# Kernel optimization log

Measured on AMD Instinct MI355X. Metric: run time of the kernel, lower is better.

The kernel has to match this reference:

```python
import jax, jax.numpy as jnp
import numpy as np

N_NODES = 100000
N_EDGES = 1600000
D = 128
RESIDUAL_WEIGHT = 0.001


def setup_inputs() -> dict:
    key = jax.random.key(0)
    k = jax.random.split(key, 7)
    x = jax.random.normal(k[0], (N_NODES, D), dtype=jnp.float32)
    edge_index = jax.random.randint(k[1], (2, N_EDGES), 0, N_NODES, dtype=jnp.int32)
    s = 1.0 / np.sqrt(D)
    Wl = jax.random.normal(k[2], (D, D), dtype=jnp.float32) * s
    bl = jax.random.normal(k[3], (D,), dtype=jnp.float32) * s
    Wr = jax.random.normal(k[4], (D, D), dtype=jnp.float32) * s
    Wres = jax.random.normal(k[5], (D, D), dtype=jnp.float32) * s
    bres = jax.random.normal(k[6], (D,), dtype=jnp.float32) * s
    return {"x": x, "edge_index": edge_index, "Wl": Wl, "bl": bl,
            "Wr": Wr, "Wres": Wres, "bres": bres}


def reference(x, edge_index, Wl, bl, Wr, Wres, bres):
    # PyG SAGEConv(aggr='sum'): messages x_j flow src -> dst
    src, dst = edge_index[0], edge_index[1]
    agg = jax.ops.segment_sum(x[src], dst, num_segments=x.shape[0])  # [N, D]
    # lin_l(agg) (with bias) + lin_r(x) (root weight, no bias)
    h_sage = agg @ Wl.T + bl + x @ Wr.T
    # residual Linear
    h_res = x @ Wres.T + bres
    rw = jnp.float32(RESIDUAL_WEIGHT)
    # dropout p=0 (eval) -> identity
    return rw * h_sage + (1.0 - rw) * h_res
```

## Files before the change

### kernel.cpp

```cpp
#include <hip/hip_runtime.h>
#include <hip/hip_bf16.h>
#include <stdint.h>

#define DD 128
#define RW 0.001f
#define CHUNK 4096
#define CAP 4096
#define YS 8.0f

#if defined(__has_builtin)
#if __has_builtin(__builtin_amdgcn_cvt_scalef32_pk_fp4_f32) && __has_builtin(__builtin_amdgcn_cvt_scalef32_pk_f32_fp4)
#define HAVE_FP4 1
#endif
#endif
#ifndef HAVE_FP4
#define HAVE_FP4 0
#endif

#if HAVE_FP4
#define XBB 64
#else
#define XBB 128
#endif

typedef __attribute__((ext_vector_type(4))) float f32x4;
typedef __attribute__((ext_vector_type(2))) float f32x2;
typedef __attribute__((ext_vector_type(8))) short bf16x8;

static __device__ __forceinline__ uint32_t pack2(float lo, float hi){
  return __builtin_amdgcn_perm(__float_as_uint(hi), __float_as_uint(lo), 0x07060302u);
}

static __device__ __forceinline__ ushort rne_bf16(float f){
  uint32_t u = __float_as_uint(f);
  return (ushort)((u + 0x7fffu + ((u >> 16) & 1u)) >> 16);
}

__global__ __launch_bounds__(512) void fused_prep(
    const int* __restrict__ src, const int* __restrict__ dst,
    int* __restrict__ gcnt, uint32_t* __restrict__ recs, int E, int nb, int nchunk,
    const float* __restrict__ x, uint8_t* __restrict__ xb, int n8, int nq, int M,
    const float* __restrict__ Wl, const float* __restrict__ bl,
    const float* __restrict__ Wr, const float* __restrict__ Wres,
    const float* __restrict__ bres, ushort* __restrict__ Wfb, float* __restrict__ bc)
{
  __shared__ uint32_t srec[CHUNK];
  __shared__ uint16_t sb[CHUNK];
  __shared__ int hcnt[800];
  __shared__ int hbase[800];
  __shared__ int lcur[800];
  int t = threadIdx.x;
  int b = blockIdx.x;

  if (b < nchunk){
    int base = b * CHUNK;
    for (int i = t; i < nb; i += 512){ hcnt[i] = 0; lcur[i] = 0; }
    __syncthreads();
    #pragma unroll
    for (int k = 0; k < 8; k++){
      int idx = k * 512 + t;
      int e = base + idx;
      uint16_t bb = 0xFFFFu;
      if (e < E){
        int d = dst[e];
        bb = (uint16_t)(d >> 7);
        srec[idx] = ((uint32_t)(d & 127) << 17) | (uint32_t)src[e];
        atomicAdd(&hcnt[bb], 1);
      }
      sb[idx] = bb;
    }
    __syncthreads();
    for (int i = t; i < nb; i += 512)
      hbase[i] = hcnt[i] ? atomicAdd(&gcnt[i], hcnt[i]) : 0;
    __syncthreads();
    #pragma unroll
    for (int k = 0; k < 8; k++){
      int idx = k * 512 + t;
      uint16_t bb = sb[idx];
      if (bb != 0xFFFFu){
        int p = hbase[bb] + atomicAdd(&lcur[bb], 1);
        if (p < CAP) recs[(size_t)bb * CAP + p] = srec[idx];
      }
    }
  } else if (b < nchunk + nq){
    int i = (b - nchunk) * 512 + t;
    if (i < n8){
      const f32x4* p = (const f32x4*)(x + (size_t)i * 8);
      f32x4 f0 = p[0], f1 = p[1];
#if HAVE_FP4
      uint32_t d = 0;
      d = __builtin_amdgcn_cvt_scalef32_pk_fp4_f32(d, f0[0], f0[1], 1.0f, 0);
      d = __builtin_amdgcn_cvt_scalef32_pk_fp4_f32(d, f0[2], f0[3], 1.0f, 1);
      d = __builtin_amdgcn_cvt_scalef32_pk_fp4_f32(d, f1[0], f1[1], 1.0f, 2);
      d = __builtin_amdgcn_cvt_scalef32_pk_fp4_f32(d, f1[2], f1[3], 1.0f, 3);
      *(uint32_t*)(xb + (size_t)i * 4) = d;
#else
      int pk0 = __builtin_amdgcn_cvt_pk_fp8_f32(f0[0], f0[1], 0, false);
      pk0     = __builtin_amdgcn_cvt_pk_fp8_f32(f0[2], f0[3], pk0, true);
      int pk1 = __builtin_amdgcn_cvt_pk_fp8_f32(f1[0], f1[1], 0, false);
      pk1     = __builtin_amdgcn_cvt_pk_fp8_f32(f1[2], f1[3], pk1, true);
      uint2 w; w.x = (uint32_t)pk0; w.y = (uint32_t)pk1;
      *(uint2*)(xb + (size_t)i * 8) = w;
#endif
    }
  } else {
    int i = (b - nchunk - nq) * 512 + t;
    if (i < 8 && i * 16 < XBB){
      uint4 z = {0u, 0u, 0u, 0u};
      *(uint4*)(xb + (size_t)M * XBB + i * 16) = z;
    }
    if (i < DD * 256){
      int c = i >> 8, k = i & 255;
      float v;
      if (k < DD) v = RW * Wr[c * DD + k] + (1.f - RW) * Wres[c * DD + k];
      else        v = (RW / YS) * Wl[c * DD + (k - DD)];
      Wfb[i] = rne_bf16(v);
      if (i < DD) bc[i] = RW * bl[i] + (1.f - RW) * bres[i];
    }
  }
}

__global__ __launch_bounds__(512) void bsort(uint32_t* __restrict__ recs,
                                             const int* __restrict__ gcnt,
                                             int2* __restrict__ meta, int M){
  __shared__ uint32_t srec[CAP];
  __shared__ uint32_t ssorted[CAP];
  __shared__ int h[128], pstart[128], lc[128];
  int t = threadIdx.x;
  int b = blockIdx.x;
  int s = b * CAP;
  int cnt = gcnt[b];
  if (cnt > CAP) cnt = CAP;

  if (t < 128){ h[t] = 0; lc[t] = 0; }
  __syncthreads();
  for (int i = t; i < cnt; i += 512){
    uint32_t r = recs[s + i];
    srec[i] = r;
    atomicAdd(&h[(r >> 17) & 127u], 1);
  }
  __syncthreads();
  int val = (t < 128) ? h[t] : 0;
  #pragma unroll
  for (int off = 1; off < 128; off <<= 1){
    if (t < 128) pstart[t] = val;
    __syncthreads();
    if (t < 128 && t >= off) val += pstart[t - off];
    __syncthreads();
  }
  if (t < 128){
    pstart[t] = val - h[t];
    int node = b * 128 + t;
    if (node < M) meta[node] = make_int2(s + pstart[t], h[t]);
  }
  __syncthreads();
  for (int i = t; i < cnt; i += 512){
    uint32_t r = srec[i];
    int n7 = (int)((r >> 17) & 127u);
    int pos = pstart[n7] + atomicAdd(&lc[n7], 1);
    ssorted[pos] = r & 0x1FFFFu;
  }
  __syncthreads();
  for (int i = t; i < cnt; i += 512)
    recs[s + i] = ssorted[i];
}

__global__ __launch_bounds__(256) void agg(const uint8_t* __restrict__ xb,
                                           const uint32_t* __restrict__ csr,
                                           const int2* __restrict__ meta,
                                           uint8_t* __restrict__ ybar, int N)
{
  int wid = (int)((blockIdx.x * 256 + threadIdx.x) >> 6);
  if (wid >= N) return;
  int lane = threadIdx.x & 63;
  int2 mc = meta[wid];
  int start = mc.x, cnt = mc.y;
  uint32_t raw = csr[start + lane];
  uint32_t vidx = (lane < cnt) ? raw : (uint32_t)N;

  f32x2 acc[8];
  #pragma unroll
  for (int k = 0; k < 8; k++) acc[k] = (f32x2){0.f, 0.f};

#if HAVE_FP4
  int voff = lane;
#else
  int voff = lane * 2;
#endif

  int n64 = cnt < 64 ? cnt : 64;
  int nit = (n64 + 15) >> 4;
  for (int it = 0; it < nit; it++){
    int bb = it << 4;
    #pragma unroll
    for (int k = 0; k < 16; k++){
      uint32_t s = (uint32_t)__builtin_amdgcn_readlane((int)vidx, bb + k);
#if HAVE_FP4
      int v = *(const uint8_t*)(xb + (size_t)s * XBB + voff);
      f32x2 f = __builtin_amdgcn_cvt_scalef32_pk_f32_fp4(v, 1.0f, 0);
#else
      int v = *(const ushort*)(xb + (size_t)s * XBB + voff);
      f32x2 f = __builtin_amdgcn_cvt_pk_f32_fp8(v, false);
#endif
      acc[k & 7] += f;
    }
  }
  for (int j = 64; j < cnt; j++){
    uint32_t s = csr[start + j];
#if HAVE_FP4
    int v = *(const uint8_t*)(xb + (size_t)s * XBB + voff);
    f32x2 f = __builtin_amdgcn_cvt_scalef32_pk_f32_fp4(v, 1.0f, 0);
#else
    int v = *(const ushort*)(xb + (size_t)s * XBB + voff);
    f32x2 f = __builtin_amdgcn_cvt_pk_f32_fp8(v, false);
#endif
    acc[0] += f;
  }

  f32x2 r = (acc[0] + acc[1]) + (acc[2] + acc[3]) + ((acc[4] + acc[5]) + (acc[6] + acc[7]));
  float a0 = r[0] * YS, a1 = r[1] * YS;
  int pk = __builtin_amdgcn_cvt_pk_fp8_f32(a0, a1, 0, false);
  *(ushort*)(ybar + (size_t)wid * DD + lane * 2) = (ushort)(pk & 0xFFFF);
}

__global__ __launch_bounds__(512, 4) void gemm2(
    const float* __restrict__ x, const uint8_t* __restrict__ ybar,
    const ushort* __restrict__ Wfb, const float* __restrict__ bc,
    float* __restrict__ out, int M)
{
  __shared__ char sX[32768];
  int tid = threadIdx.x;
  int lane = tid & 63, w = tid >> 6;
  int wr = w >> 2, wcol = w & 3;
  int l15 = lane & 15, lhi = lane >> 4;
  int rowbase = blockIdx.x * 128 + wr * 64;
  int colbase = wcol * 32;

  f32x4 acc[4][2];
  #pragma unroll
  for (int a = 0; a < 4; a++)
    #pragma unroll
    for (int b = 0; b < 2; b++) acc[a][b] = (f32x4){0.f,0.f,0.f,0.f};

  #pragma unroll
  for (int p = 0; p < 4; p++){
    int g   = p * 512 + tid;
    int row = g >> 4;
    int cx  = tid & 15;
    int grow = blockIdx.x * 128 + row;
    if (grow >= M) grow = M - 1;
    const float* ap = x + (size_t)grow * DD + cx * 8;
    f32x4 f0 = *(const f32x4*)ap;
    f32x4 f1 = *(const f32x4*)(ap + 4);
    uint4 wv;
    wv.x = pack2(f0[0], f0[1]);
    wv.y = pack2(f0[2], f0[3]);
    wv.z = pack2(f1[0], f1[1]);
    wv.w = pack2(f1[2], f1[3]);
    int sw = (row << 8) | ((cx * 16) ^ ((row & 7) << 4));
    *(uint4*)&sX[sw] = wv;
  }
  __syncthreads();

  #pragma unroll
  for (int ks = 0; ks < 4; ks++){
    bf16x8 afr[4];
    #pragma unroll
    for (int rt = 0; rt < 4; rt++){
      int row = wr * 64 + rt * 16 + l15;
      int byte = (row << 8) | ((ks * 64 + lhi * 16) ^ ((row & 7) << 4));
      afr[rt] = *(const bf16x8*)&sX[byte];
    }
    #pragma unroll
    for (int ct = 0; ct < 2; ct++){
      int colm = colbase + ct * 16 + l15;
      bf16x8 bfr = *(const bf16x8*)(Wfb + (size_t)colm * 256 + ks * 32 + lhi * 8);
      #pragma unroll
      for (int rt = 0; rt < 4; rt++)
        acc[rt][ct] = __builtin_amdgcn_mfma_f32_16x16x32_bf16(bfr, afr[rt], acc[rt][ct], 0, 0, 0);
    }
  }
  __syncthreads();

  #pragma unroll
  for (int p = 0; p < 4; p++){
    int g   = p * 512 + tid;
    int row = g >> 4;
    int cx  = tid & 15;
    int grow = blockIdx.x * 128 + row;
    if (grow >= M) grow = M - 1;
    uint2 rv = *(const uint2*)(ybar + (size_t)grow * DD + cx * 8);
    f32x2 e0 = __builtin_amdgcn_cvt_pk_f32_fp8((int)rv.x, false);
    f32x2 e1 = __builtin_amdgcn_cvt_pk_f32_fp8((int)rv.x, true);
    f32x2 e2 = __builtin_amdgcn_cvt_pk_f32_fp8((int)rv.y, false);
    f32x2 e3 = __builtin_amdgcn_cvt_pk_f32_fp8((int)rv.y, true);
    uint4 wv;
    wv.x = pack2(e0[0], e0[1]);
    wv.y = pack2(e1[0], e1[1]);
    wv.z = pack2(e2[0], e2[1]);
    wv.w = pack2(e3[0], e3[1]);
    int sw = (row << 8) | ((cx * 16) ^ ((row & 7) << 4));
    *(uint4*)&sX[sw] = wv;
  }
  __syncthreads();

  #pragma unroll
  for (int ks = 0; ks < 4; ks++){
    bf16x8 afr[4];
    #pragma unroll
    for (int rt = 0; rt < 4; rt++){
      int row = wr * 64 + rt * 16 + l15;
      int byte = (row << 8) | ((ks * 64 + lhi * 16) ^ ((row & 7) << 4));
      afr[rt] = *(const bf16x8*)&sX[byte];
    }
    #pragma unroll
    for (int ct = 0; ct < 2; ct++){
      int colm = colbase + ct * 16 + l15;
      bf16x8 bfr = *(const bf16x8*)(Wfb + (size_t)colm * 256 + 128 + ks * 32 + lhi * 8);
      #pragma unroll
      for (int rt = 0; rt < 4; rt++)
        acc[rt][ct] = __builtin_amdgcn_mfma_f32_16x16x32_bf16(bfr, afr[rt], acc[rt][ct], 0, 0, 0);
    }
  }

  #pragma unroll
  for (int ct = 0; ct < 2; ct++){
    int col = colbase + ct * 16 + lhi * 4;
    f32x4 b4 = *(const f32x4*)&bc[col];
    #pragma unroll
    for (int rt = 0; rt < 4; rt++){
      int row = rowbase + rt * 16 + l15;
      if (row < M){
        f32x4 o = acc[rt][ct] + b4;
        *(f32x4*)(out + (size_t)row * DD + col) = o;
      }
    }
  }
}

extern "C" void kernel_launch(void* const* d_in, const int* in_sizes, int n_in,
                              void* d_out, int out_size, void* d_ws, size_t ws_size,
                              hipStream_t stream) {
  const float* x    = (const float*)d_in[0];
  const int*   ei   = (const int*)d_in[1];
  const float* Wl   = (const float*)d_in[2];
  const float* bl   = (const float*)d_in[3];
  const float* Wr   = (const float*)d_in[4];
  const float* Wres = (const float*)d_in[5];
  const float* bres = (const float*)d_in[6];
  float* out = (float*)d_out;

  int M = in_sizes[0] / DD;
  int E = in_sizes[1] / 2;
  const int* esrc = ei;
  const int* edst = ei + E;
  int nb = (M + 127) >> 7;

  char* wsp = (char*)d_ws;
  size_t off = 0;
  uint8_t*  xb   = (uint8_t*) (wsp + off); off += (size_t)(M + 1) * 128; off = (off + 255) & ~255ull;
  uint8_t*  ybar = (uint8_t*) (wsp + off); off += (size_t)M * DD;        off = (off + 255) & ~255ull;
  uint32_t* recs = (uint32_t*)(wsp + off); off += (size_t)800 * CAP * 4;
  ushort*   Wfb  = (ushort*)  (wsp + off); off += DD * 256 * 2;
  float*    bc   = (float*)   (wsp + off); off += 512;
  int*      gcnt = (int*)     (wsp + off); off += sizeof(int) * 1024;
  int2*     meta = (int2*)    (wsp + off); off += sizeof(int2) * (size_t)M;

  int n8 = M * 16;
  int nchunk = (E + CHUNK - 1) / CHUNK;
  int nq = (n8 + 511) / 512;
  int nprep = (DD * 256 + 511) / 512;

  hipMemsetAsync(gcnt, 0, sizeof(int) * 1024, stream);
  fused_prep<<<nchunk + nq + nprep, 512, 0, stream>>>(
      esrc, edst, gcnt, recs, E, nb, nchunk,
      x, xb, n8, nq, M,
      Wl, bl, Wr, Wres, bres, Wfb, bc);
  bsort<<<nb, 512, 0, stream>>>(recs, gcnt, meta, M);
  agg<<<((size_t)M * 64 + 255) / 256, 256, 0, stream>>>(xb, recs, meta, ybar, M);
  gemm2<<<(M + 127) / 128, 512, 0, stream>>>(x, ybar, Wfb, bc, out, M);
}
```

Before: 111.2 us.

## Fuse neighbor aggregation into the GEMM kernel, dropping the fp8 ybar buffer

The separate aggregation kernel is removed. Each GEMM block now gathers neighbor sums for its own 128 nodes directly into shared memory as bf16, with each wave handling 16 nodes and prefetching the next node's CSR entries. This removes a kernel launch and the write-then-read round trip of the fp8 ybar intermediate, along with its YS scaling. The cost is that gather latency now runs inside the GEMM block, with fewer waves per node and only two accumulators instead of eight. Occupancy hints are raised to 6 blocks per CU to help hide that latency.

```diff
diff --git a/kernel.cpp b/kernel.cpp
--- a/kernel.cpp
+++ b/kernel.cpp
@@ -6,7 +6,6 @@
 #define RW 0.001f
 #define CHUNK 4096
 #define CAP 4096
-#define YS 8.0f
 
 #if defined(__has_builtin)
 #if __has_builtin(__builtin_amdgcn_cvt_scalef32_pk_fp4_f32) && __has_builtin(__builtin_amdgcn_cvt_scalef32_pk_f32_fp4)
@@ -113,7 +112,7 @@
       int c = i >> 8, k = i & 255;
       float v;
       if (k < DD) v = RW * Wr[c * DD + k] + (1.f - RW) * Wres[c * DD + k];
-      else        v = (RW / YS) * Wl[c * DD + (k - DD)];
+      else        v = RW * Wl[c * DD + (k - DD)];
       Wfb[i] = rne_bf16(v);
       if (i < DD) bc[i] = RW * bl[i] + (1.f - RW) * bres[i];
     }
@@ -165,72 +164,76 @@
     recs[s + i] = ssorted[i];
 }
 
-__global__ __launch_bounds__(256) void agg(const uint8_t* __restrict__ xb,
-                                           const uint32_t* __restrict__ csr,
-                                           const int2* __restrict__ meta,
-                                           uint8_t* __restrict__ ybar, int N)
-{
-  int wid = (int)((blockIdx.x * 256 + threadIdx.x) >> 6);
-  if (wid >= N) return;
-  int lane = threadIdx.x & 63;
-  int2 mc = meta[wid];
-  int start = mc.x, cnt = mc.y;
-  uint32_t raw = csr[start + lane];
-  uint32_t vidx = (lane < cnt) ? raw : (uint32_t)N;
-
-  f32x2 acc[8];
-  #pragma unroll
-  for (int k = 0; k < 8; k++) acc[k] = (f32x2){0.f, 0.f};
-
-#if HAVE_FP4
-  int voff = lane;
-#else
-  int voff = lane * 2;
-#endif
-
-  int n64 = cnt < 64 ? cnt : 64;
-  int nit = (n64 + 15) >> 4;
-  for (int it = 0; it < nit; it++){
-    int bb = it << 4;
-    #pragma unroll
-    for (int k = 0; k < 16; k++){
-      uint32_t s = (uint32_t)__builtin_amdgcn_readlane((int)vidx, bb + k);
-#if HAVE_FP4
-      int v = *(const uint8_t*)(xb + (size_t)s * XBB + voff);
-      f32x2 f = __builtin_amdgcn_cvt_scalef32_pk_f32_fp4(v, 1.0f, 0);
-#else
-      int v = *(const ushort*)(xb + (size_t)s * XBB + voff);
-      f32x2 f = __builtin_amdgcn_cvt_pk_f32_fp8(v, false);
-#endif
-      acc[k & 7] += f;
-    }
-  }
-  for (int j = 64; j < cnt; j++){
-    uint32_t s = csr[start + j];
-#if HAVE_FP4
-    int v = *(const uint8_t*)(xb + (size_t)s * XBB + voff);
-    f32x2 f = __builtin_amdgcn_cvt_scalef32_pk_f32_fp4(v, 1.0f, 0);
-#else
-    int v = *(const ushort*)(xb + (size_t)s * XBB + voff);
-    f32x2 f = __builtin_amdgcn_cvt_pk_f32_fp8(v, false);
-#endif
-    acc[0] += f;
-  }
-
-  f32x2 r = (acc[0] + acc[1]) + (acc[2] + acc[3]) + ((acc[4] + acc[5]) + (acc[6] + acc[7]));
-  float a0 = r[0] * YS, a1 = r[1] * YS;
-  int pk = __builtin_amdgcn_cvt_pk_fp8_f32(a0, a1, 0, false);
-  *(ushort*)(ybar + (size_t)wid * DD + lane * 2) = (ushort)(pk & 0xFFFF);
-}
-
-__global__ __launch_bounds__(512, 4) void gemm2(
-    const float* __restrict__ x, const uint8_t* __restrict__ ybar,
+__global__ __launch_bounds__(512, 6) void gemm_agg(
+    const float* __restrict__ x, const uint8_t* __restrict__ xb,
+    const uint32_t* __restrict__ csr, const int2* __restrict__ meta,
     const ushort* __restrict__ Wfb, const float* __restrict__ bc,
     float* __restrict__ out, int M)
 {
   __shared__ char sX[32768];
   int tid = threadIdx.x;
   int lane = tid & 63, w = tid >> 6;
+
+  {
+    int nodebase = blockIdx.x * 128 + w * 16;
+    int mrow = nodebase + (lane & 15);
+    int2 mpre = (mrow < M) ? meta[mrow] : make_int2(0, 0);
+
+    int start = __builtin_amdgcn_readlane(mpre.x, 0);
+    int cnt   = __builtin_amdgcn_readlane(mpre.y, 0);
+    uint32_t vidx = csr[start + lane];
+    vidx = (lane < cnt) ? vidx : (uint32_t)M;
+
+    for (int j = 0; j < 16; j++){
+      int start_n = 0, cnt_n = 0;
+      uint32_t vidx_n = (uint32_t)M;
+      if (j < 15){
+        start_n = __builtin_amdgcn_readlane(mpre.x, j + 1);
+        cnt_n   = __builtin_amdgcn_readlane(mpre.y, j + 1);
+        uint32_t rawn = csr[start_n + lane];
+        vidx_n = (lane < cnt_n) ? rawn : (uint32_t)M;
+      }
+
+      f32x2 acc0 = (f32x2){0.f, 0.f}, acc1 = (f32x2){0.f, 0.f};
+      int n64 = cnt < 64 ? cnt : 64;
+      int nit = (n64 + 15) >> 4;
+      for (int it = 0; it < nit; it++){
+        int bb = it << 4;
+        #pragma unroll
+        for (int k = 0; k < 16; k++){
+          uint32_t s = (uint32_t)__builtin_amdgcn_readlane((int)vidx, bb + k);
+#if HAVE_FP4
+          int v = *(const uint8_t*)(xb + (size_t)s * XBB + lane);
+          f32x2 f = __builtin_amdgcn_cvt_scalef32_pk_f32_fp4(v, 1.0f, 0);
+#else
+          int v = *(const ushort*)(xb + (size_t)s * XBB + lane * 2);
+          f32x2 f = __builtin_amdgcn_cvt_pk_f32_fp8(v, false);
+#endif
+          if (k & 1) acc1 += f; else acc0 += f;
+        }
+      }
+      for (int t2 = 64; t2 < cnt; t2++){
+        uint32_t s = csr[start + t2];
+#if HAVE_FP4
+        int v = *(const uint8_t*)(xb + (size_t)s * XBB + lane);
+        f32x2 f = __builtin_amdgcn_cvt_scalef32_pk_f32_fp4(v, 1.0f, 0);
+#else
+        int v = *(const ushort*)(xb + (size_t)s * XBB + lane * 2);
+        f32x2 f = __builtin_amdgcn_cvt_pk_f32_fp8(v, false);
+#endif
+        acc0 += f;
+      }
+      f32x2 acc = acc0 + acc1;
+
+      int row = w * 16 + j;
+      int sw = (row << 8) | ((lane * 4) ^ ((row & 7) << 4));
+      *(uint32_t*)&sX[sw] = pack2(acc[0], acc[1]);
+
+      start = start_n; cnt = cnt_n; vidx = vidx_n;
+    }
+  }
+  __syncthreads();
+
   int wr = w >> 2, wcol = w & 3;
   int l15 = lane & 15, lhi = lane >> 4;
   int rowbase = blockIdx.x * 128 + wr * 64;
@@ -241,6 +244,26 @@
   for (int a = 0; a < 4; a++)
     #pragma unroll
     for (int b = 0; b < 2; b++) acc[a][b] = (f32x4){0.f,0.f,0.f,0.f};
+
+  #pragma unroll
+  for (int ks = 0; ks < 4; ks++){
+    bf16x8 afr[4];
+    #pragma unroll
+    for (int rt = 0; rt < 4; rt++){
+      int row = wr * 64 + rt * 16 + l15;
+      int byte = (row << 8) | ((ks * 64 + lhi * 16) ^ ((row & 7) << 4));
+      afr[rt] = *(const bf16x8*)&sX[byte];
+    }
+    #pragma unroll
+    for (int ct = 0; ct < 2; ct++){
+      int colm = colbase + ct * 16 + l15;
+      bf16x8 bfr = *(const bf16x8*)(Wfb + (size_t)colm * 256 + 128 + ks * 32 + lhi * 8);
+      #pragma unroll
+      for (int rt = 0; rt < 4; rt++)
+        acc[rt][ct] = __builtin_amdgcn_mfma_f32_16x16x32_bf16(bfr, afr[rt], acc[rt][ct], 0, 0, 0);
+    }
+  }
+  __syncthreads();
 
   #pragma unroll
   for (int p = 0; p < 4; p++){
@@ -280,48 +303,6 @@
         acc[rt][ct] = __builtin_amdgcn_mfma_f32_16x16x32_bf16(bfr, afr[rt], acc[rt][ct], 0, 0, 0);
     }
   }
-  __syncthreads();
-
-  #pragma unroll
-  for (int p = 0; p < 4; p++){
-    int g   = p * 512 + tid;
-    int row = g >> 4;
-    int cx  = tid & 15;
-    int grow = blockIdx.x * 128 + row;
-    if (grow >= M) grow = M - 1;
-    uint2 rv = *(const uint2*)(ybar + (size_t)grow * DD + cx * 8);
-    f32x2 e0 = __builtin_amdgcn_cvt_pk_f32_fp8((int)rv.x, false);
-    f32x2 e1 = __builtin_amdgcn_cvt_pk_f32_fp8((int)rv.x, true);
-    f32x2 e2 = __builtin_amdgcn_cvt_pk_f32_fp8((int)rv.y, false);
-    f32x2 e3 = __builtin_amdgcn_cvt_pk_f32_fp8((int)rv.y, true);
-    uint4 wv;
-    wv.x = pack2(e0[0], e0[1]);
-    wv.y = pack2(e1[0], e1[1]);
-    wv.z = pack2(e2[0], e2[1]);
-    wv.w = pack2(e3[0], e3[1]);
-    int sw = (row << 8) | ((cx * 16) ^ ((row & 7) << 4));
-    *(uint4*)&sX[sw] = wv;
-  }
-  __syncthreads();
-
-  #pragma unroll
-  for (int ks = 0; ks < 4; ks++){
-    bf16x8 afr[4];
-    #pragma unroll
-    for (int rt = 0; rt < 4; rt++){
-      int row = wr * 64 + rt * 16 + l15;
-      int byte = (row << 8) | ((ks * 64 + lhi * 16) ^ ((row & 7) << 4));
-      afr[rt] = *(const bf16x8*)&sX[byte];
-    }
-    #pragma unroll
-    for (int ct = 0; ct < 2; ct++){
-      int colm = colbase + ct * 16 + l15;
-      bf16x8 bfr = *(const bf16x8*)(Wfb + (size_t)colm * 256 + 128 + ks * 32 + lhi * 8);
-      #pragma unroll
-      for (int rt = 0; rt < 4; rt++)
-        acc[rt][ct] = __builtin_amdgcn_mfma_f32_16x16x32_bf16(bfr, afr[rt], acc[rt][ct], 0, 0, 0);
-    }
-  }
 
   #pragma unroll
   for (int ct = 0; ct < 2; ct++){
@@ -359,7 +340,6 @@
   char* wsp = (char*)d_ws;
   size_t off = 0;
   uint8_t*  xb   = (uint8_t*) (wsp + off); off += (size_t)(M + 1) * 128; off = (off + 255) & ~255ull;
-  uint8_t*  ybar = (uint8_t*) (wsp + off); off += (size_t)M * DD;        off = (off + 255) & ~255ull;
   uint32_t* recs = (uint32_t*)(wsp + off); off += (size_t)800 * CAP * 4;
   ushort*   Wfb  = (ushort*)  (wsp + off); off += DD * 256 * 2;
   float*    bc   = (float*)   (wsp + off); off += 512;
@@ -377,6 +357,5 @@
       x, xb, n8, nq, M,
       Wl, bl, Wr, Wres, bres, Wfb, bc);
   bsort<<<nb, 512, 0, stream>>>(recs, gcnt, meta, M);
-  agg<<<((size_t)M * 64 + 255) / 256, 256, 0, stream>>>(xb, recs, meta, ybar, M);
-  gemm2<<<(M + 127) / 128, 512, 0, stream>>>(x, ybar, Wfb, bc, out, M);
-}
+  gemm_agg<<<nb, 512, 0, stream>>>(x, xb, recs, meta, Wfb, bc, out, M);
+}
```

Result: slower. 118.8 us (+6.8%).
